# Optimization experiments

Hardware: AMD Instinct MI355X
Metric: run time of the kernel (lower is better)

## Reference

```python
import jax, jax.numpy as jnp
import numpy as np

H, W, C = 384, 384, 200
HIDE, CNN_OUT, NCLS = 128, 64, 16
N = H * W
E = 1179648
EPS = 1e-5  # torch BatchNorm eps


def _bn(x, g, b, axes):
    # training-mode batch norm (biased variance), matches torch BN in train mode
    m = x.mean(axes, keepdims=True)
    v = x.var(axes, keepdims=True)
    return (x - m) * jax.lax.rsqrt(v + EPS) * g + b


def _gcn(x, w, bias, src, dst, n):
    # PyG GCNConv: add self loops, symmetric D^-1/2 (A+I) D^-1/2 normalization
    h = x @ w  # [N, out]
    loop = jnp.arange(n, dtype=src.dtype)
    s = jnp.concatenate([src, loop])
    d = jnp.concatenate([dst, loop])
    deg = jax.ops.segment_sum(jnp.ones(s.shape, x.dtype), d, num_segments=n)
    dinv = jnp.where(deg > 0, jax.lax.rsqrt(jnp.maximum(deg, 1.0)) * (deg > 0), 0.0)
    norm = dinv[s] * dinv[d]  # [E+N]
    out = jax.ops.segment_sum(h[s] * norm[:, None], d, num_segments=n)
    return out + bias


def _gnn_layer(x, bn_g, bn_b, w, b, src, dst):
    # F.normalize (row L2) -> BN1d -> GCNConv -> LeakyReLU (dropout off in eval)
    nrm = jnp.linalg.norm(x, axis=1, keepdims=True)
    x = x / jnp.maximum(nrm, 1e-12)
    x = _bn(x, bn_g, bn_b, (0,))
    return jax.nn.leaky_relu(_gcn(x, w, b, src, dst, x.shape[0]))


def setup_inputs() -> dict:
    key = jax.random.key(0)
    ks = jax.random.split(key, 16)
    p = {}
    p["x"] = jax.random.normal(ks[0], (H, W, C), jnp.float32)
    p["edge_index"] = jax.random.randint(ks[1], (2, E), 0, N, jnp.int32)
    # CNN_denoise: BN(C) -> 1x1 conv C->128 -> BN(128) -> 1x1 conv 128->128
    p["dn_bn1_g"] = jnp.ones((C,), jnp.float32); p["dn_bn1_b"] = jnp.zeros((C,), jnp.float32)
    p["dn_w1"] = jax.random.normal(ks[2], (C, HIDE), jnp.float32) * 0.05
    p["dn_b1"] = jnp.zeros((HIDE,), jnp.float32)
    p["dn_bn2_g"] = jnp.ones((HIDE,), jnp.float32); p["dn_bn2_b"] = jnp.zeros((HIDE,), jnp.float32)
    p["dn_w2"] = jax.random.normal(ks[3], (HIDE, HIDE), jnp.float32) * 0.05
    p["dn_b2"] = jnp.zeros((HIDE,), jnp.float32)
    # CNNCONV(128,64,k=5): BN(128) -> point 1x1 128->64 (no bias) -> depthwise 5x5 (bias)
    p["cnn_bn_g"] = jnp.ones((HIDE,), jnp.float32); p["cnn_bn_b"] = jnp.zeros((HIDE,), jnp.float32)
    p["cnn_pw"] = jax.random.normal(ks[4], (HIDE, CNN_OUT), jnp.float32) * 0.05
    p["cnn_dw"] = jax.random.normal(ks[5], (CNN_OUT, 1, 5, 5), jnp.float32) * 0.05
    p["cnn_db"] = jnp.zeros((CNN_OUT,), jnp.float32)
    # GCN branch: GNN(128,128), GNN(128,128), GNN(128,64)
    dims = [(HIDE, HIDE), (HIDE, HIDE), (HIDE, CNN_OUT)]
    for i, (di, do) in enumerate(dims, 1):
        p[f"g{i}_bn_g"] = jnp.ones((di,), jnp.float32)
        p[f"g{i}_bn_b"] = jnp.zeros((di,), jnp.float32)
        p[f"g{i}_w"] = jax.random.normal(ks[5 + i], (di, do), jnp.float32) * 0.05
        p[f"g{i}_b"] = jnp.zeros((do,), jnp.float32)
    p["lin_w"] = jax.random.normal(ks[9], (HIDE, NCLS), jnp.float32) * 0.05
    p["lin_b"] = jnp.zeros((NCLS,), jnp.float32)
    return p


def reference(x, edge_index,
              dn_bn1_g, dn_bn1_b, dn_w1, dn_b1, dn_bn2_g, dn_bn2_b, dn_w2, dn_b2,
              cnn_bn_g, cnn_bn_b, cnn_pw, cnn_dw, cnn_db,
              g1_bn_g, g1_bn_b, g1_w, g1_b,
              g2_bn_g, g2_bn_b, g2_w, g2_b,
              g3_bn_g, g3_bn_b, g3_w, g3_b,
              lin_w, lin_b):
    src, dst = edge_index[0], edge_index[1]
    # CNN_denoise (channel-last; 1x1 convs are matmuls)
    h = _bn(x, dn_bn1_g, dn_bn1_b, (0, 1))
    h = jax.nn.leaky_relu(h @ dn_w1 + dn_b1)
    h = _bn(h, dn_bn2_g, dn_bn2_b, (0, 1))
    clean = jax.nn.leaky_relu(h @ dn_w2 + dn_b2)       # [H,W,128]
    flat = clean.reshape(N, HIDE)
    # CNN branch: BN -> 1x1 -> LeakyReLU -> depthwise 5x5 -> LeakyReLU
    c = _bn(clean, cnn_bn_g, cnn_bn_b, (0, 1))
    c = jax.nn.leaky_relu(c @ cnn_pw)                  # [H,W,64]
    cn = c.transpose(2, 0, 1)[None]                    # [1,64,H,W]
    cn = jax.lax.conv_general_dilated(
        cn, cnn_dw, (1, 1), 'SAME', feature_group_count=CNN_OUT,
        dimension_numbers=('NCHW', 'OIHW', 'NCHW'))
    cn = jax.nn.leaky_relu(cn[0].transpose(1, 2, 0) + cnn_db)
    cnn_res = cn.reshape(N, CNN_OUT)
    # GCN branch (3 layers)
    g = _gnn_layer(flat, g1_bn_g, g1_bn_b, g1_w, g1_b, src, dst)
    g = _gnn_layer(g, g2_bn_g, g2_bn_b, g2_w, g2_b, src, dst)
    g = _gnn_layer(g, g3_bn_g, g3_bn_b, g3_w, g3_b, src, dst)
    y = jnp.concatenate([g, cnn_res], axis=-1) @ lin_w + lin_b
    return jax.nn.softmax(y, axis=-1)
```

## Files before the change

### kernel.cpp

```cpp
#include <hip/hip_runtime.h>
#include <stddef.h>

#define HH 384
#define WW 384
#define CC 200
#define NN 147456
#define EE 1179648
#define HIDE 128
#define COUT 64
#define NCLS 16
#define BN_EPS 1e-5f

#define SREP 16
#define SLOTF (512 * SREP)
#define DBINS 64

using u16 = unsigned short;
typedef __attribute__((ext_vector_type(8))) short short8;
typedef __attribute__((ext_vector_type(4))) float float4v;

__device__ __forceinline__ float b2f(u16 u) {
    union { unsigned int i; float f; } v; v.i = ((unsigned int)u) << 16; return v.f;
}
__device__ __forceinline__ u16 f2b(float f) {
    union { float f; unsigned int i; } v; v.f = f;
    unsigned int x = v.i;
    unsigned int r = (x + 0x7fffu + ((x >> 16) & 1u)) >> 16;
    return (u16)r;
}
__device__ __forceinline__ float lrelu(float v) { return v > 0.f ? v : 0.01f * v; }

__global__ void sniff(const u16* __restrict__ x, int* __restrict__ flag) {
    __shared__ int cntS;
    if (threadIdx.x == 0) cntS = 0;
    __syncthreads();
    int c = 0;
    for (int i = 0; i < 8; i++) {
        u16 h = x[threadIdx.x * 8 + i];
        int hb = (h >> 8) & 0x7F;
        if (hb >= 0x3C && hb <= 0x41) c++;
    }
    atomicAdd(&cntS, c);
    __syncthreads();
    if (threadIdx.x == 0) *flag = (cntS < 1536) ? 1 : 0;
}

#define NPAR 27
struct PConv { const void* src[NPAR]; int n[NPAR]; int off[NPAR]; };

__global__ void convert_params(PConv pc, const int* __restrict__ flag,
                               u16* __restrict__ dst) {
    int b = blockIdx.x;
    int n = pc.n[b];
    const void* s = pc.src[b];
    u16* d = dst + pc.off[b];
    int isf = *flag;
    if (isf) {
        const float* sf = (const float*)s;
        for (int i = threadIdx.x; i < n; i += 256) d[i] = f2b(sf[i]);
    } else {
        const u16* sh = (const u16*)s;
        for (int i = threadIdx.x; i < n; i += 256) d[i] = sh[i];
    }
}

__global__ __launch_bounds__(256) void stats200(const void* __restrict__ X,
                                                const int* __restrict__ flag,
                                                float* __restrict__ arena) {
    __shared__ __align__(16) u16 s[128 * 200];
    int t = threadIdx.x;
    int r0 = blockIdx.x * 128;
    if (*flag) {
        const float* Xf = (const float*)X;
        for (int i = t; i < 128 * 25; i += 256) {
            int r = i / 25, kc = i - r * 25;
            const float* p = Xf + (size_t)(r0 + r) * CC + kc * 8;
            float4v a = *(const float4v*)p;
            float4v b = *(const float4v*)(p + 4);
            short8 v;
            #pragma unroll
            for (int j = 0; j < 4; j++) { v[j] = (short)f2b(a[j]); v[4 + j] = (short)f2b(b[j]); }
            *(short8*)&s[r * 200 + kc * 8] = v;
        }
    } else {
        const u16* Xh = (const u16*)X;
        for (int i = t; i < 128 * 25; i += 256) {
            int r = i / 25, kc = i - r * 25;
            *(short8*)&s[r * 200 + kc * 8] =
                *(const short8*)(Xh + (size_t)(r0 + r) * CC + kc * 8);
        }
    }
    __syncthreads();
    if (t < CC) {
        float sum = 0.f, sq = 0.f;
        for (int r = 0; r < 128; r++) {
            float v = b2f(s[r * 200 + t]);
            sum += v; sq += v * v;
        }
        float* rep = arena + (blockIdx.x & (SREP - 1)) * 512;
        atomicAdd(&rep[t], sum);
        atomicAdd(&rep[256 + t], sq);
    }
}

template<int K, int KPAD, int O>
__global__ __launch_bounds__(256) void fold_bn(
        const float* __restrict__ arena, float invN,
        const u16* __restrict__ bng, const u16* __restrict__ bnb,
        const u16* __restrict__ Wsrc, const u16* __restrict__ extrab,
        u16* __restrict__ WT, float* __restrict__ cb) {
    __shared__ float aS[KPAD], sS[KPAD];
    int t = threadIdx.x;
    if (t < KPAD) {
        float a = 0.f, sh = 0.f;
        if (t < K) {
            float sum = 0.f, sq = 0.f;
            #pragma unroll
            for (int r = 0; r < SREP; r++) {
                sum += arena[r * 512 + t];
                sq  += arena[r * 512 + 256 + t];
            }
            float m = sum * invN;
            float var = fmaxf(sq * invN - m * m, 0.f);
            a = b2f(bng[t]) * rsqrtf(var + BN_EPS);
            sh = b2f(bnb[t]) - m * a;
        }
        aS[t] = a; sS[t] = sh;
    }
    __syncthreads();
    int g = t >> 6, l = t & 63;
    int o = blockIdx.x * 4 + g;
    if (o < O) {
        float c = 0.f;
        #pragma unroll
        for (int k = l; k < KPAD; k += 64) {
            float w = (k < K) ? b2f(Wsrc[k * O + o]) : 0.f;
            c += sS[k] * w;
            WT[o * KPAD + k] = f2b(aS[k] * w);
        }
        #pragma unroll
        for (int s = 32; s >= 1; s >>= 1) c += __shfl_down(c, s);
        if (l == 0) cb[o] = c + (extrab ? b2f(extrab[o]) : 0.f);
    }
}

template<int KT, int KSRC, int O, bool LEAKY, bool SCALE, int STATS, bool DUAL>
__global__ __launch_bounds__(256) void gemm_mfma(
        const void* __restrict__ Ap, const u16* __restrict__ WT,
        const float* __restrict__ cb, const float* __restrict__ s1,
        const float* __restrict__ s2, const int* __restrict__ f32p,
        u16* __restrict__ out, float* __restrict__ stA,
        float* __restrict__ stB, float* __restrict__ invn,
        u16* __restrict__ out2) {
    constexpr int KPAD = KT * 32;
    constexpr int LDA = KPAD + 8;
    constexpr int CHR = KPAD / 8;
    constexpr int CHD = KSRC / 8;
    constexpr int NCT = O / 16;
    constexpr int CPW = NCT / 4;
    __shared__ __align__(16) u16 As[64 * LDA];
    __shared__ float rS[4][64];
    __shared__ float invS[64];
    __shared__ float sS1[64], sS2[64];
    int tid = threadIdx.x;
    int row0 = blockIdx.x * 64;

    int isf = f32p ? *f32p : 0;
    if (isf) {
        const float* A = (const float*)Ap;
        for (int i = tid; i < 64 * CHR; i += 256) {
            int r = i / CHR, kc = i - r * CHR;
            short8 v = {0, 0, 0, 0, 0, 0, 0, 0};
            if (kc < CHD) {
                const float* p = A + (size_t)(row0 + r) * KSRC + kc * 8;
                float4v a = *(const float4v*)p;
                float4v b = *(const float4v*)(p + 4);
                #pragma unroll
                for (int j = 0; j < 4; j++) { v[j] = (short)f2b(a[j]); v[4 + j] = (short)f2b(b[j]); }
            }
            *(short8*)&As[r * LDA + kc * 8] = v;
        }
    } else {
        const u16* A = (const u16*)Ap;
        for (int i = tid; i < 64 * CHR; i += 256) {
            int r = i / CHR, kc = i - r * CHR;
            short8 v = {0, 0, 0, 0, 0, 0, 0, 0};
            if (kc < CHD)
                v = *(const short8*)(A + (size_t)(row0 + r) * KSRC + kc * 8);
            *(short8*)&As[r * LDA + kc * 8] = v;
        }
    }
    if (SCALE && tid < 64) { sS1[tid] = s1[row0 + tid]; sS2[tid] = s2[row0 + tid]; }
    __syncthreads();

    int w = tid >> 6, lane = tid & 63, m = lane & 15, q = lane >> 4;
    float4v acc[4][CPW];
    #pragma unroll
    for (int mf = 0; mf < 4; mf++)
        #pragma unroll
        for (int cp = 0; cp < CPW; cp++)
            acc[mf][cp] = (float4v){0.f, 0.f, 0.f, 0.f};

    const u16* Abp = &As[m * LDA + q * 8];
    const u16* Bbp = WT + (size_t)((w * CPW) * 16 + m) * KPAD + q * 8;

    #pragma unroll
    for (int kt = 0; kt < KT; kt++) {
        short8 af[4];
        #pragma unroll
        for (int mf = 0; mf < 4; mf++)
            af[mf] = *(const short8*)(Abp + mf * 16 * LDA + kt * 32);
        #pragma unroll
        for (int cp = 0; cp < CPW; cp++) {
            short8 bf = *(const short8*)(Bbp + (size_t)cp * 16 * KPAD + kt * 32);
            #pragma unroll
            for (int mf = 0; mf < 4; mf++)
                acc[mf][cp] = __builtin_amdgcn_mfma_f32_16x16x32_bf16(
                    af[mf], bf, acc[mf][cp], 0, 0, 0);
        }
    }

    float rp[4][4] = {};
    #pragma unroll
    for (int cp = 0; cp < CPW; cp++) {
        int ct = w * CPW + cp;
        int col = ct * 16 + m;
        float cbv = cb[col];
        #pragma unroll
        for (int mf = 0; mf < 4; mf++) {
            #pragma unroll
            for (int r = 0; r < 4; r++) {
                int rl = mf * 16 + q * 4 + r;
                float x = acc[mf][cp][r];
                if constexpr (DUAL) {
                    if (ct < 8) {
                        x = (x * sS1[rl] + cbv) * sS2[rl];
                        out[(size_t)(row0 + rl) * 128 + col] = f2b(x);
                    } else {
                        x = lrelu(x + cbv);
                        out2[(size_t)(row0 + rl) * 64 + (col - 128)] = f2b(x);
                    }
                } else {
                    if constexpr (SCALE) x = (x * sS1[rl] + cbv) * sS2[rl];
                    else                 x += cbv;
                    if constexpr (LEAKY) x = lrelu(x);
                    out[(size_t)(row0 + rl) * O + col] = f2b(x);
                }
                acc[mf][cp][r] = x;
                if constexpr (STATS == 2) rp[mf][r] += x * x;
            }
        }
    }

    if constexpr (STATS == 2) {
        #pragma unroll
        for (int mf = 0; mf < 4; mf++) {
            #pragma unroll
            for (int r = 0; r < 4; r++) {
                float v = rp[mf][r];
                v += __shfl_xor(v, 1); v += __shfl_xor(v, 2);
                v += __shfl_xor(v, 4); v += __shfl_xor(v, 8);
                if (m == 0) rS[w][mf * 16 + q * 4 + r] = v;
            }
        }
        __syncthreads();
        if (tid < 64) {
            float ss = rS[0][tid] + rS[1][tid] + rS[2][tid] + rS[3][tid];
            float inv = 1.0f / fmaxf(sqrtf(ss), 1e-12f);
            invS[tid] = inv;
            invn[row0 + tid] = inv;
        }
        __syncthreads();
    }

    if constexpr (STATS >= 1) {
        float* stAr = stA + (blockIdx.x & (SREP - 1)) * 512;
        float* stBr = (STATS == 2) ? stB + (blockIdx.x & (SREP - 1)) * 512 : nullptr;
        #pragma unroll
        for (int cp = 0; cp < CPW; cp++) {
            int col = (w * CPW + cp) * 16 + m;
            float cs = 0.f, cq = 0.f, ns = 0.f, nq = 0.f;
            #pragma unroll
            for (int mf = 0; mf < 4; mf++) {
                #pragma unroll
                for (int r = 0; r < 4; r++) {
                    float x = acc[mf][cp][r];
                    cs += x; cq += x * x;
                    if constexpr (STATS == 2) {
                        float nv = x * invS[mf * 16 + q * 4 + r];
                        ns += nv; nq += nv * nv;
                    }
                }
            }
            cs += __shfl_xor(cs, 16); cs += __shfl_xor(cs, 32);
            cq += __shfl_xor(cq, 16); cq += __shfl_xor(cq, 32);
            if constexpr (STATS == 2) {
                ns += __shfl_xor(ns, 16); ns += __shfl_xor(ns, 32);
                nq += __shfl_xor(nq, 16); nq += __shfl_xor(nq, 32);
            }
            if (q == 0) {
                atomicAdd(&stAr[col], cs);
                atomicAdd(&stAr[256 + col], cq);
                if constexpr (STATS == 2) {
                    atomicAdd(&stBr[col], ns);
                    atomicAdd(&stBr[256 + col], nq);
                }
            }
        }
    }
}

__global__ void hist(const int* __restrict__ dst, int* __restrict__ cnt) {
    int e = blockIdx.x * 256 + threadIdx.x;
    unsigned d = (unsigned)dst[e];
    if (d < (unsigned)NN) atomicAdd(&cnt[d], 1);
}
__global__ void mkdinv(const int* __restrict__ cnt, float* __restrict__ dinv) {
    int i = blockIdx.x * 256 + threadIdx.x;
    int c = cnt[i]; if (c < 0) c = 0;
    dinv[i] = rsqrtf((float)c + 1.0f);
}
__global__ void scan_part(const int* __restrict__ cnt, int* __restrict__ bsum) {
    int b = blockIdx.x, t = threadIdx.x;
    int base = b * 1024 + t * 4;
    int s = cnt[base] + cnt[base + 1] + cnt[base + 2] + cnt[base + 3];
    #pragma unroll
    for (int o = 32; o >= 1; o >>= 1) s += __shfl_down(s, o);
    __shared__ int ws4[4];
    if ((t & 63) == 0) ws4[t >> 6] = s;
    __syncthreads();
    if (t == 0) bsum[b] = ws4[0] + ws4[1] + ws4[2] + ws4[3];
}
__global__ void scan_top(const int* __restrict__ bsum, int* __restrict__ boff) {
    if (threadIdx.x == 0) {
        int a = 0;
        for (int i = 0; i < 144; i++) { boff[i] = a; a += bsum[i]; }
    }
}
__global__ void scan_write(const int* __restrict__ cnt, const int* __restrict__ boff,
                           int* __restrict__ offv) {
    int b = blockIdx.x, t = threadIdx.x;
    int base = b * 1024 + t * 4;
    int v0 = cnt[base], v1 = cnt[base + 1], v2 = cnt[base + 2], v3 = cnt[base + 3];
    int ts = v0 + v1 + v2 + v3;
    __shared__ int sc[256];
    sc[t] = ts;
    __syncthreads();
    for (int o = 1; o < 256; o <<= 1) {
        int x = (t >= o) ? sc[t - o] : 0;
        __syncthreads();
        sc[t] += x;
        __syncthreads();
    }
    int excl = boff[b] + sc[t] - ts;
    offv[base] = excl;
    offv[base + 1] = excl + v0;
    offv[base + 2] = excl + v0 + v1;
    offv[base + 3] = excl + v0 + v1 + v2;
    if (b == 143 && t == 255) offv[NN] = excl + ts;
}
__global__ void scatter(const int* __restrict__ src, const int* __restrict__ dst,
                        int* __restrict__ cursor, const int* __restrict__ offv,
                        int* __restrict__ csr) {
    int e = blockIdx.x * 256 + threadIdx.x;
    unsigned d = (unsigned)dst[e];
    if (d >= (unsigned)NN) return;
    int p = atomicAdd(&cursor[d], 1);
    unsigned idx = (unsigned)(offv[d] + p);
    if (idx < (unsigned)EE) csr[idx] = src[e];
}

__global__ void deg_hist(const int* __restrict__ cnt, int* __restrict__ dbin) {
    __shared__ int h[DBINS];
    int t = threadIdx.x;
    if (t < DBINS) h[t] = 0;
    __syncthreads();
    int i = blockIdx.x * 256 + t;
    int dg = cnt[i]; if (dg < 0) dg = 0; if (dg > DBINS - 1) dg = DBINS - 1;
    atomicAdd(&h[dg], 1);
    __syncthreads();
    if (t < DBINS) atomicAdd(&dbin[t], h[t]);
}
__global__ void deg_scan(const int* __restrict__ dbin, int* __restrict__ dbase) {
    if (threadIdx.x == 0) {
        int a = 0;
        for (int b = DBINS - 1; b >= 0; b--) { dbase[b] = a; a += dbin[b]; }
    }
}
__global__ void deg_scatter(const int* __restrict__ cnt, int* __restrict__ dbase,
                            int* __restrict__ perm) {
    __shared__ int h[DBINS], base[DBINS];
    int t = threadIdx.x;
    if (t < DBINS) h[t] = 0;
    __syncthreads();
    int i = blockIdx.x * 256 + t;
    int dg = cnt[i]; if (dg < 0) dg = 0; if (dg > DBINS - 1) dg = DBINS - 1;
    atomicAdd(&h[dg], 1);
    __syncthreads();
    if (t < DBINS) { base[t] = atomicAdd(&dbase[t], h[t]); h[t] = 0; }
    __syncthreads();
    int lp = atomicAdd(&h[dg], 1);
    perm[base[dg] + lp] = i;
}

template<int O, int STATS, int GRP>
__global__ __launch_bounds__(256) void aggregate(
        const u16* __restrict__ h2, const int* __restrict__ offv,
        const int* __restrict__ csr, const float* __restrict__ dinv,
        const u16* __restrict__ gb, u16* __restrict__ outp,
        float* __restrict__ stA, float* __restrict__ invn,
        const int* __restrict__ perm) {
    constexpr int CH = O / 8;
    constexpr int NPB = 256 / CH;
    __shared__ float colS[O], colQ[O];
    int t = threadIdx.x;
    if (STATS && t < O) { colS[t] = 0.f; colQ[t] = 0.f; }
    int local = t / CH, c = t % CH;
    size_t cof = (size_t)c * 8;
    const u16* hb = h2 + cof;
    short8 gv = *(const short8*)(gb + cof);
    float sreg[8] = {0.f, 0.f, 0.f, 0.f, 0.f, 0.f, 0.f, 0.f};
    float qreg[8] = {0.f, 0.f, 0.f, 0.f, 0.f, 0.f, 0.f, 0.f};

    #pragma unroll
    for (int g = 0; g < GRP; g++) {
        int pos = blockIdx.x * (NPB * GRP) + g * NPB + local;
        int d = perm[pos];
        float acc[8];
        short8 selfv = *(const short8*)(hb + (size_t)d * O);
        #pragma unroll
        for (int j = 0; j < 8; j++) acc[j] = b2f((u16)selfv[j]);
        int e0 = offv[d], e1 = offv[d + 1];
        if (e0 < 0) e0 = 0;
        if (e1 > EE) e1 = EE;
        int k = e0;
        for (; k + 8 <= e1; k += 8) {
            unsigned i0 = (unsigned)csr[k],     i1 = (unsigned)csr[k + 1];
            unsigned i2 = (unsigned)csr[k + 2], i3 = (unsigned)csr[k + 3];
            unsigned i4 = (unsigned)csr[k + 4], i5 = (unsigned)csr[k + 5];
            unsigned i6 = (unsigned)csr[k + 6], i7 = (unsigned)csr[k + 7];
            short8 v0 = *(const short8*)(hb + (size_t)i0 * O);
            short8 v1 = *(const short8*)(hb + (size_t)i1 * O);
            short8 v2 = *(const short8*)(hb + (size_t)i2 * O);
            short8 v3 = *(const short8*)(hb + (size_t)i3 * O);
            short8 v4 = *(const short8*)(hb + (size_t)i4 * O);
            short8 v5 = *(const short8*)(hb + (size_t)i5 * O);
            short8 v6 = *(const short8*)(hb + (size_t)i6 * O);
            short8 v7 = *(const short8*)(hb + (size_t)i7 * O);
            #pragma unroll
            for (int j = 0; j < 8; j++)
                acc[j] += ((b2f((u16)v0[j]) + b2f((u16)v1[j])) +
                           (b2f((u16)v2[j]) + b2f((u16)v3[j]))) +
                          ((b2f((u16)v4[j]) + b2f((u16)v5[j])) +
                           (b2f((u16)v6[j]) + b2f((u16)v7[j])));
        }
        if (k + 4 <= e1) {
            unsigned i0 = (unsigned)csr[k],     i1 = (unsigned)csr[k + 1];
            unsigned i2 = (unsigned)csr[k + 2], i3 = (unsigned)csr[k + 3];
            short8 v0 = *(const short8*)(hb + (size_t)i0 * O);
            short8 v1 = *(const short8*)(hb + (size_t)i1 * O);
            short8 v2 = *(const short8*)(hb + (size_t)i2 * O);
            short8 v3 = *(const short8*)(hb + (size_t)i3 * O);
            #pragma unroll
            for (int j = 0; j < 8; j++)
                acc[j] += (b2f((u16)v0[j]) + b2f((u16)v1[j])) +
                          (b2f((u16)v2[j]) + b2f((u16)v3[j]));
            k += 4;
        }
        if (k + 2 <= e1) {
            unsigned i0 = (unsigned)csr[k], i1 = (unsigned)csr[k + 1];
            short8 v0 = *(const short8*)(hb + (size_t)i0 * O);
            short8 v1 = *(const short8*)(hb + (size_t)i1 * O);
            #pragma unroll
            for (int j = 0; j < 8; j++)
                acc[j] += b2f((u16)v0[j]) + b2f((u16)v1[j]);
            k += 2;
        }
        if (k < e1) {
            unsigned i0 = (unsigned)csr[k];
            short8 v0 = *(const short8*)(hb + (size_t)i0 * O);
            #pragma unroll
            for (int j = 0; j < 8; j++) acc[j] += b2f((u16)v0[j]);
        }
        float dd = dinv[d];
        float outv[8];
        short8 res;
        #pragma unroll
        for (int j = 0; j < 8; j++) {
            outv[j] = lrelu(dd * acc[j] + b2f((u16)gv[j]));
            res[j] = (short)f2b(outv[j]);
        }
        *(short8*)(outp + (size_t)d * O + cof) = res;

        if constexpr (STATS) {
            float ss = 0.f;
            #pragma unroll
            for (int j = 0; j < 8; j++) ss += outv[j] * outv[j];
            ss += __shfl_xor(ss, 1); ss += __shfl_xor(ss, 2);
            ss += __shfl_xor(ss, 4); ss += __shfl_xor(ss, 8);
            float inv = 1.0f / fmaxf(sqrtf(ss), 1e-12f);
            if (c == 0) invn[d] = inv;
            #pragma unroll
            for (int j = 0; j < 8; j++) {
                float nv = outv[j] * inv;
                sreg[j] += nv; qreg[j] += nv * nv;
            }
        }
    }

    if constexpr (STATS) {
        __syncthreads();
        #pragma unroll
        for (int j = 0; j < 8; j++) {
            float s = sreg[j];
            s += __shfl_xor(s, 16); s += __shfl_xor(s, 32);
            float qq = qreg[j];
            qq += __shfl_xor(qq, 16); qq += __shfl_xor(qq, 32);
            if ((t & 63) < 16) {
                atomicAdd(&colS[c * 8 + j], s);
                atomicAdd(&colQ[c * 8 + j], qq);
            }
        }
        __syncthreads();
        if (t < O) {
            float* rep = stA + (blockIdx.x & (SREP - 1)) * 512;
            atomicAdd(&rep[t], colS[t]);
            atomicAdd(&rep[256 + t], colQ[t]);
        }
    }
}

__global__ __launch_bounds__(256) void final_fused(
        const u16* __restrict__ g3, const u16* __restrict__ cpre,
        const u16* __restrict__ dwW, const u16* __restrict__ db,
        const u16* __restrict__ lw, const u16* __restrict__ lb,
        const int* __restrict__ flag, void* __restrict__ outp) {
    __shared__ __align__(16) u16 tile[400 * 72];
    __shared__ __align__(16) u16 wT[25 * 64];
    __shared__ __align__(16) u16 wL[2048];
    __shared__ float bDW[64];
    __shared__ float bL[16];
    int t = threadIdx.x;
    int tx = blockIdx.x % 24, ty = blockIdx.x / 24;
    int x0 = tx * 16 - 2, y0 = ty * 16 - 2;
    for (int i = t; i < 1600; i += 256) {
        int f = i / 25, tap = i - f * 25;
        wT[tap * 64 + f] = dwW[i];
    }
    for (int i = t; i < 2048; i += 256) wL[i] = lw[i];
    if (t < 64) bDW[t] = b2f(db[t]);
    if (t < 16) bL[t] = b2f(lb[t]);
    for (int u = t; u < 3200; u += 256) {
        int pix = u >> 3, c8 = u & 7;
        int gy = y0 + pix / 20, gx = x0 + pix % 20;
        short8 v = {0, 0, 0, 0, 0, 0, 0, 0};
        if (gy >= 0 && gy < HH && gx >= 0 && gx < WW)
            v = *(const short8*)(cpre + ((size_t)(gy * WW + gx)) * 64 + c8 * 8);
        *(short8*)&tile[pix * 72 + c8 * 8] = v;
    }
    __syncthreads();

    int px = t & 15, py = t >> 4;
    int node = (ty * 16 + py) * WW + tx * 16 + px;
    float y[16];
    #pragma unroll
    for (int o = 0; o < 16; o++) y[o] = bL[o];

    const u16* g3p = g3 + (size_t)node * 64;
    for (int c8 = 0; c8 < 8; c8++) {
        short8 gvv = *(const short8*)(g3p + c8 * 8);
        #pragma unroll
        for (int j = 0; j < 8; j++) {
            float g = b2f((u16)gvv[j]);
            const short8 w0 = *(const short8*)&wL[(c8 * 8 + j) * 16];
            const short8 w1 = *(const short8*)&wL[(c8 * 8 + j) * 16 + 8];
            #pragma unroll
            for (int o = 0; o < 8; o++) {
                y[o]     += g * b2f((u16)w0[o]);
                y[o + 8] += g * b2f((u16)w1[o]);
            }
        }
    }
    for (int c8 = 0; c8 < 8; c8++) {
        float acc[8] = {0.f, 0.f, 0.f, 0.f, 0.f, 0.f, 0.f, 0.f};
        #pragma unroll
        for (int dy = 0; dy < 5; dy++) {
            int rbase = ((py + dy) * 20 + px) * 72 + c8 * 8;
            #pragma unroll
            for (int dx = 0; dx < 5; dx++) {
                short8 v  = *(const short8*)&tile[rbase + dx * 72];
                short8 wv = *(const short8*)&wT[(dy * 5 + dx) * 64 + c8 * 8];
                #pragma unroll
                for (int j = 0; j < 8; j++)
                    acc[j] += b2f((u16)v[j]) * b2f((u16)wv[j]);
            }
        }
        #pragma unroll
        for (int j = 0; j < 8; j++) {
            float cv = lrelu(acc[j] + bDW[c8 * 8 + j]);
            int f = 64 + c8 * 8 + j;
            const short8 w0 = *(const short8*)&wL[f * 16];
            const short8 w1 = *(const short8*)&wL[f * 16 + 8];
            #pragma unroll
            for (int o = 0; o < 8; o++) {
                y[o]     += cv * b2f((u16)w0[o]);
                y[o + 8] += cv * b2f((u16)w1[o]);
            }
        }
    }
    float mx = y[0];
    #pragma unroll
    for (int o = 1; o < 16; o++) mx = fmaxf(mx, y[o]);
    float sum = 0.f;
    #pragma unroll
    for (int o = 0; o < 16; o++) { y[o] = __expf(y[o] - mx); sum += y[o]; }
    float inv = 1.0f / fmaxf(sum, 1e-30f);
    if (*flag) {
        float* of = (float*)outp;
        #pragma unroll
        for (int o = 0; o < 16; o++) of[(size_t)node * 16 + o] = y[o] * inv;
    } else {
        u16* oh = (u16*)outp;
        #pragma unroll
        for (int o = 0; o < 16; o++) oh[(size_t)node * 16 + o] = f2b(y[o] * inv);
    }
}

extern "C" void kernel_launch(void* const* d_in, const int* in_sizes, int n_in,
                              void* d_out, int out_size, void* d_ws, size_t ws_size,
                              hipStream_t stream) {
    const void* X   = d_in[0];
    const int* EIDX = (const int*)d_in[1];
    const int* esrc = EIDX;
    const int* edst = EIDX + EE;

    char* ws = (char*)d_ws;
    size_t off = 0;
    auto alloc = [&](size_t sz) -> char* {
        size_t szr = (sz + 255) & ~(size_t)255;
        char* p;
        if (off + szr <= ws_size) { p = ws + off; off += szr; }
        else { p = ws; }
        return p;
    };

    int*   dflag   = (int*)alloc(256);
    static const int pidx[NPAR] = {2,3,4,5,6,7,8,9,10,11,12,13,14,
                                   15,16,17,18,19,20,21,22,23,24,25,26,27,28};
    static const int pn[NPAR]   = {200,200,25600,128,128,128,16384,128,
                                   128,128,8192,1600,64,
                                   128,128,16384,128,
                                   128,128,16384,128,
                                   128,128,8192,64,
                                   2048,16};
    u16* parena = (u16*)alloc(100352 * 2);
    PConv pc;
    {
        int po = 0;
        for (int i = 0; i < NPAR; i++) {
            pc.src[i] = d_in[pidx[i]];
            pc.n[i] = pn[i];
            pc.off[i] = po;
            po += (pn[i] + 15) & ~15;
        }
    }
    const u16* DN1G = parena + pc.off[0];
    const u16* DN1B = parena + pc.off[1];
    const u16* DNW1 = parena + pc.off[2];
    const u16* DNB1 = parena + pc.off[3];
    const u16* DN2G = parena + pc.off[4];
    const u16* DN2B = parena + pc.off[5];
    const u16* DNW2 = parena + pc.off[6];
    const u16* DNB2 = parena + pc.off[7];
    const u16* CBNG = parena + pc.off[8];
    const u16* CBNB = parena + pc.off[9];
    const u16* CPW  = parena + pc.off[10];
    const u16* CDW  = parena + pc.off[11];
    const u16* CDB  = parena + pc.off[12];
    const u16* G1G  = parena + pc.off[13];
    const u16* G1B  = parena + pc.off[14];
    const u16* G1W  = parena + pc.off[15];
    const u16* G1BI = parena + pc.off[16];
    const u16* G2G  = parena + pc.off[17];
    const u16* G2B  = parena + pc.off[18];
    const u16* G2W  = parena + pc.off[19];
    const u16* G2BI = parena + pc.off[20];
    const u16* G3G  = parena + pc.off[21];
    const u16* G3B  = parena + pc.off[22];
    const u16* G3W  = parena + pc.off[23];
    const u16* G3BI = parena + pc.off[24];
    const u16* LINW = parena + pc.off[25];
    const u16* LINB = parena + pc.off[26];

    int*   cnt     = (int*)alloc((size_t)NN * 4);
    int*   cursor  = (int*)alloc((size_t)NN * 4);
    float* arena   = (float*)alloc((size_t)6 * SLOTF * 4);
    int*   dbin    = (int*)alloc(DBINS * 4);
    int*   offv    = (int*)alloc((size_t)(NN + 1) * 4);
    int*   bsum    = (int*)alloc(144 * 4);
    int*   boff    = (int*)alloc(144 * 4);
    int*   dbase   = (int*)alloc(DBINS * 4);
    int*   perm    = (int*)alloc((size_t)NN * 4);
    float* dinvp   = (float*)alloc((size_t)NN * 4);
    float* invnorm = (float*)alloc((size_t)NN * 4);
    u16*   W1T     = (u16*)alloc(128 * 224 * 2);
    u16*   W2T     = (u16*)alloc(128 * 128 * 2);
    u16*   WgT     = (u16*)alloc(192 * 128 * 2);
    float* cb1     = (float*)alloc(128 * 4);
    float* cb2     = (float*)alloc(128 * 4);
    float* cbg     = (float*)alloc(192 * 4);
    int*   csr     = (int*)alloc((size_t)EE * 4);
    u16*   cbuf    = (u16*)alloc((size_t)NN * 64 * 2);
    u16*   big1    = (u16*)alloc((size_t)NN * 128 * 2);
    u16*   big2    = (u16*)alloc((size_t)NN * 128 * 2);

    const float invN = 1.0f / (float)NN;
    size_t zsz = (size_t)((char*)dbin + 256 - (char*)cnt);
    size_t zcap = ((char*)cnt >= ws && (size_t)((char*)cnt - ws) < ws_size)
                      ? ws_size - (size_t)((char*)cnt - ws) : 0;
    if (zsz > zcap) zsz = zcap;
    hipMemsetAsync(cnt, 0, zsz, stream);

    sniff<<<1, 256, 0, stream>>>((const u16*)X, dflag);
    convert_params<<<NPAR, 256, 0, stream>>>(pc, dflag, parena);

    hist<<<EE / 256, 256, 0, stream>>>(edst, cnt);
    mkdinv<<<NN / 256, 256, 0, stream>>>(cnt, dinvp);
    deg_hist<<<NN / 256, 256, 0, stream>>>(cnt, dbin);
    deg_scan<<<1, 64, 0, stream>>>(dbin, dbase);
    deg_scatter<<<NN / 256, 256, 0, stream>>>(cnt, dbase, perm);
    scan_part<<<144, 256, 0, stream>>>(cnt, bsum);
    scan_top<<<1, 64, 0, stream>>>(bsum, boff);
    scan_write<<<144, 256, 0, stream>>>(cnt, boff, offv);
    scatter<<<EE / 256, 256, 0, stream>>>(esrc, edst, cursor, offv, csr);

    stats200<<<1152, 256, 0, stream>>>(X, dflag, arena + 0 * SLOTF);
    fold_bn<200, 224, 128><<<32, 256, 0, stream>>>(arena + 0 * SLOTF, invN, DN1G, DN1B, DNW1, DNB1, W1T, cb1);
    gemm_mfma<7, 200, 128, true, false, 1, false><<<NN / 64, 256, 0, stream>>>(
        X, W1T, cb1, nullptr, nullptr, dflag, big1, arena + 1 * SLOTF, nullptr, nullptr, nullptr);
    fold_bn<128, 128, 128><<<32, 256, 0, stream>>>(arena + 1 * SLOTF, invN, DN2G, DN2B, DNW2, DNB2, W2T, cb2);
    gemm_mfma<4, 128, 128, true, false, 2, false><<<NN / 64, 256, 0, stream>>>(
        big1, W2T, cb2, nullptr, nullptr, nullptr, big2, arena + 2 * SLOTF, arena + 3 * SLOTF, invnorm, nullptr);

    fold_bn<128, 128, 128><<<32, 256, 0, stream>>>(arena + 3 * SLOTF, invN, G1G, G1B, G1W, nullptr, WgT, cbg);
    fold_bn<128, 128, 64><<<16, 256, 0, stream>>>(arena + 2 * SLOTF, invN, CBNG, CBNB, CPW, nullptr,
                                                  WgT + 128 * 128, cbg + 128);
    gemm_mfma<4, 128, 192, false, true, 0, true><<<NN / 64, 256, 0, stream>>>(
        big2, WgT, cbg, invnorm, dinvp, nullptr, big1, nullptr, nullptr, nullptr, cbuf);
    aggregate<128, 1, 4><<<NN / 64, 256, 0, stream>>>(
        big1, offv, csr, dinvp, G1BI, big2, arena + 4 * SLOTF, invnorm, perm);

    fold_bn<128, 128, 128><<<32, 256, 0, stream>>>(arena + 4 * SLOTF, invN, G2G, G2B, G2W, nullptr, WgT, cbg);
    gemm_mfma<4, 128, 128, false, true, 0, false><<<NN / 64, 256, 0, stream>>>(
        big2, WgT, cbg, invnorm, dinvp, nullptr, big1, nullptr, nullptr, nullptr, nullptr);
    aggregate<128, 1, 4><<<NN / 64, 256, 0, stream>>>(
        big1, offv, csr, dinvp, G2BI, big2, arena + 5 * SLOTF, invnorm, perm);

    fold_bn<128, 128, 64><<<16, 256, 0, stream>>>(arena + 5 * SLOTF, invN, G3G, G3B, G3W, nullptr, WgT, cbg);
    gemm_mfma<4, 128, 64, false, true, 0, false><<<NN / 64, 256, 0, stream>>>(
        big2, WgT, cbg, invnorm, dinvp, nullptr, big1, nullptr, nullptr, nullptr, nullptr);
    aggregate<64, 0, 1><<<NN / 32, 256, 0, stream>>>(
        big1, offv, csr, dinvp, G3BI, big2, nullptr, nullptr, perm);

    final_fused<<<576, 256, 0, stream>>>(big2, cbuf, CDW, CDB, LINW, LINB, dflag, d_out);

    (void)in_sizes; (void)n_in; (void)out_size;
}
```

Before: 798.7 us.

## Build CSR via two-level bucket partition with LDS-local counting instead of global atomics

Replaces the global-atomic histogram, three-kernel scan and global-atomic scatter with a bucketed counting sort. Edges are first partitioned by destination into 72 buckets of 2048 nodes using per-block shared-memory counters, then each bucket builds its CSR offsets and column lists with LDS atomics. Degrees for dinv and the degree-sort permutation are derived from offset differences. This removes contended global atomics and random global writes, but adds an 8-byte-per-edge intermediate pass, and csr_build runs as only 72 blocks, which limits parallelism.

Result: faster. 760.1 us (-4.8%).

```diff
diff --git a/kernel.cpp b/kernel.cpp
--- a/kernel.cpp
+++ b/kernel.cpp
@@ -14,6 +14,10 @@
 #define SREP 16
 #define SLOTF (512 * SREP)
 #define DBINS 64
+
+#define NBKT 72
+#define NPBK 288
+#define EPB  4096
 
 using u16 = unsigned short;
 typedef __attribute__((ext_vector_type(8))) short short8;
@@ -310,73 +314,122 @@
     }
 }
 
-__global__ void hist(const int* __restrict__ dst, int* __restrict__ cnt) {
-    int e = blockIdx.x * 256 + threadIdx.x;
-    unsigned d = (unsigned)dst[e];
-    if (d < (unsigned)NN) atomicAdd(&cnt[d], 1);
-}
-__global__ void mkdinv(const int* __restrict__ cnt, float* __restrict__ dinv) {
+__global__ __launch_bounds__(256) void count_bkt(const int* __restrict__ edst,
+                                                 int* __restrict__ counts) {
+    __shared__ int h[NBKT];
+    int t = threadIdx.x, blk = blockIdx.x;
+    if (t < NBKT) h[t] = 0;
+    __syncthreads();
+    int base = blk * EPB;
+    for (int i = t; i < EPB; i += 256) {
+        unsigned d = (unsigned)edst[base + i];
+        if (d < (unsigned)NN) atomicAdd(&h[d >> 11], 1);
+    }
+    __syncthreads();
+    if (t < NBKT) counts[t * NPBK + blk] = h[t];
+}
+
+__global__ void scan_bkt(int* __restrict__ counts, int* __restrict__ bbase) {
+    __shared__ int bs[NBKT], bb[NBKT];
+    int t = threadIdx.x;
+    if (t < NBKT) {
+        int s = 0;
+        for (int i = 0; i < NPBK; i++) s += counts[t * NPBK + i];
+        bs[t] = s;
+    }
+    __syncthreads();
+    if (t == 0) {
+        int a = 0;
+        for (int b = 0; b < NBKT; b++) { bb[b] = a; bbase[b] = a; a += bs[b]; }
+        bbase[NBKT] = a;
+    }
+    __syncthreads();
+    if (t < NBKT) {
+        int run = bb[t];
+        for (int i = 0; i < NPBK; i++) {
+            int c = counts[t * NPBK + i];
+            counts[t * NPBK + i] = run;
+            run += c;
+        }
+    }
+}
+
+__global__ __launch_bounds__(256) void part_bkt(const int* __restrict__ esrc,
+                                                const int* __restrict__ edst,
+                                                const int* __restrict__ counts,
+                                                int2* __restrict__ bpair) {
+    __shared__ int cur[NBKT];
+    int t = threadIdx.x, blk = blockIdx.x;
+    if (t < NBKT) cur[t] = counts[t * NPBK + blk];
+    __syncthreads();
+    int base = blk * EPB;
+    for (int i = t; i < EPB; i += 256) {
+        unsigned d = (unsigned)edst[base + i];
+        if (d < (unsigned)NN) {
+            int pos = atomicAdd(&cur[d >> 11], 1);
+            int2 p; p.x = esrc[base + i]; p.y = (int)d;
+            bpair[pos] = p;
+        }
+    }
+}
+
+__global__ __launch_bounds__(256) void csr_build(const int2* __restrict__ bpair,
+                                                 const int* __restrict__ bbase,
+                                                 int* __restrict__ offv,
+                                                 int* __restrict__ csr) {
+    __shared__ int cntL[2048];
+    __shared__ int exL[2048];
+    __shared__ int tsum[256];
+    int b = blockIdx.x, t = threadIdx.x;
+    int e0 = bbase[b], e1 = bbase[b + 1];
+    int n0 = b << 11;
+    for (int i = t; i < 2048; i += 256) cntL[i] = 0;
+    __syncthreads();
+    for (int k = e0 + t; k < e1; k += 256) {
+        int2 p = bpair[k];
+        atomicAdd(&cntL[p.y & 2047], 1);
+    }
+    __syncthreads();
+    int s = 0;
+    #pragma unroll
+    for (int j = 0; j < 8; j++) s += cntL[t * 8 + j];
+    tsum[t] = s;
+    __syncthreads();
+    for (int o = 1; o < 256; o <<= 1) {
+        int x = (t >= o) ? tsum[t - o] : 0;
+        __syncthreads();
+        tsum[t] += x;
+        __syncthreads();
+    }
+    int run = tsum[t] - s;
+    #pragma unroll
+    for (int j = 0; j < 8; j++) { int c = cntL[t * 8 + j]; exL[t * 8 + j] = run; run += c; }
+    __syncthreads();
+    for (int i = t; i < 2048; i += 256) offv[n0 + i] = e0 + exL[i];
+    if (b == NBKT - 1 && t == 0) offv[NN] = e1;
+    for (int i = t; i < 2048; i += 256) cntL[i] = 0;
+    __syncthreads();
+    for (int k = e0 + t; k < e1; k += 256) {
+        int2 p = bpair[k];
+        int l = p.y & 2047;
+        int pos = e0 + exL[l] + atomicAdd(&cntL[l], 1);
+        csr[pos] = p.x;
+    }
+}
+
+__global__ void mkdinv2(const int* __restrict__ offv, float* __restrict__ dinv) {
     int i = blockIdx.x * 256 + threadIdx.x;
-    int c = cnt[i]; if (c < 0) c = 0;
-    dinv[i] = rsqrtf((float)c + 1.0f);
-}
-__global__ void scan_part(const int* __restrict__ cnt, int* __restrict__ bsum) {
-    int b = blockIdx.x, t = threadIdx.x;
-    int base = b * 1024 + t * 4;
-    int s = cnt[base] + cnt[base + 1] + cnt[base + 2] + cnt[base + 3];
-    #pragma unroll
-    for (int o = 32; o >= 1; o >>= 1) s += __shfl_down(s, o);
-    __shared__ int ws4[4];
-    if ((t & 63) == 0) ws4[t >> 6] = s;
-    __syncthreads();
-    if (t == 0) bsum[b] = ws4[0] + ws4[1] + ws4[2] + ws4[3];
-}
-__global__ void scan_top(const int* __restrict__ bsum, int* __restrict__ boff) {
-    if (threadIdx.x == 0) {
-        int a = 0;
-        for (int i = 0; i < 144; i++) { boff[i] = a; a += bsum[i]; }
-    }
-}
-__global__ void scan_write(const int* __restrict__ cnt, const int* __restrict__ boff,
-                           int* __restrict__ offv) {
-    int b = blockIdx.x, t = threadIdx.x;
-    int base = b * 1024 + t * 4;
-    int v0 = cnt[base], v1 = cnt[base + 1], v2 = cnt[base + 2], v3 = cnt[base + 3];
-    int ts = v0 + v1 + v2 + v3;
-    __shared__ int sc[256];
-    sc[t] = ts;
-    __syncthreads();
-    for (int o = 1; o < 256; o <<= 1) {
-        int x = (t >= o) ? sc[t - o] : 0;
-        __syncthreads();
-        sc[t] += x;
-        __syncthreads();
-    }
-    int excl = boff[b] + sc[t] - ts;
-    offv[base] = excl;
-    offv[base + 1] = excl + v0;
-    offv[base + 2] = excl + v0 + v1;
-    offv[base + 3] = excl + v0 + v1 + v2;
-    if (b == 143 && t == 255) offv[NN] = excl + ts;
-}
-__global__ void scatter(const int* __restrict__ src, const int* __restrict__ dst,
-                        int* __restrict__ cursor, const int* __restrict__ offv,
-                        int* __restrict__ csr) {
-    int e = blockIdx.x * 256 + threadIdx.x;
-    unsigned d = (unsigned)dst[e];
-    if (d >= (unsigned)NN) return;
-    int p = atomicAdd(&cursor[d], 1);
-    unsigned idx = (unsigned)(offv[d] + p);
-    if (idx < (unsigned)EE) csr[idx] = src[e];
-}
-
-__global__ void deg_hist(const int* __restrict__ cnt, int* __restrict__ dbin) {
+    dinv[i] = rsqrtf((float)(offv[i + 1] - offv[i]) + 1.0f);
+}
+
+__global__ void deg_hist(const int* __restrict__ offv, int* __restrict__ dbin) {
     __shared__ int h[DBINS];
     int t = threadIdx.x;
     if (t < DBINS) h[t] = 0;
     __syncthreads();
     int i = blockIdx.x * 256 + t;
-    int dg = cnt[i]; if (dg < 0) dg = 0; if (dg > DBINS - 1) dg = DBINS - 1;
+    int dg = offv[i + 1] - offv[i];
+    if (dg < 0) dg = 0; if (dg > DBINS - 1) dg = DBINS - 1;
     atomicAdd(&h[dg], 1);
     __syncthreads();
     if (t < DBINS) atomicAdd(&dbin[t], h[t]);
@@ -387,14 +440,15 @@
         for (int b = DBINS - 1; b >= 0; b--) { dbase[b] = a; a += dbin[b]; }
     }
 }
-__global__ void deg_scatter(const int* __restrict__ cnt, int* __restrict__ dbase,
+__global__ void deg_scatter(const int* __restrict__ offv, int* __restrict__ dbase,
                             int* __restrict__ perm) {
     __shared__ int h[DBINS], base[DBINS];
     int t = threadIdx.x;
     if (t < DBINS) h[t] = 0;
     __syncthreads();
     int i = blockIdx.x * 256 + t;
-    int dg = cnt[i]; if (dg < 0) dg = 0; if (dg > DBINS - 1) dg = DBINS - 1;
+    int dg = offv[i + 1] - offv[i];
+    if (dg < 0) dg = 0; if (dg > DBINS - 1) dg = DBINS - 1;
     atomicAdd(&h[dg], 1);
     __syncthreads();
     if (t < DBINS) { base[t] = atomicAdd(&dbase[t], h[t]); h[t] = 0; }
@@ -692,13 +746,12 @@
     const u16* LINW = parena + pc.off[25];
     const u16* LINB = parena + pc.off[26];
 
-    int*   cnt     = (int*)alloc((size_t)NN * 4);
-    int*   cursor  = (int*)alloc((size_t)NN * 4);
     float* arena   = (float*)alloc((size_t)6 * SLOTF * 4);
     int*   dbin    = (int*)alloc(DBINS * 4);
+    int*   counts  = (int*)alloc((size_t)NBKT * NPBK * 4);
+    int*   bbase   = (int*)alloc((NBKT + 1) * 4);
+    int2*  bpair   = (int2*)alloc((size_t)EE * 8);
     int*   offv    = (int*)alloc((size_t)(NN + 1) * 4);
-    int*   bsum    = (int*)alloc(144 * 4);
-    int*   boff    = (int*)alloc(144 * 4);
     int*   dbase   = (int*)alloc(DBINS * 4);
     int*   perm    = (int*)alloc((size_t)NN * 4);
     float* dinvp   = (float*)alloc((size_t)NN * 4);
@@ -715,24 +768,23 @@
     u16*   big2    = (u16*)alloc((size_t)NN * 128 * 2);
 
     const float invN = 1.0f / (float)NN;
-    size_t zsz = (size_t)((char*)dbin + 256 - (char*)cnt);
-    size_t zcap = ((char*)cnt >= ws && (size_t)((char*)cnt - ws) < ws_size)
-                      ? ws_size - (size_t)((char*)cnt - ws) : 0;
+    size_t zsz = (size_t)((char*)dbin + 256 - (char*)arena);
+    size_t zcap = ((char*)arena >= ws && (size_t)((char*)arena - ws) < ws_size)
+                      ? ws_size - (size_t)((char*)arena - ws) : 0;
     if (zsz > zcap) zsz = zcap;
-    hipMemsetAsync(cnt, 0, zsz, stream);
+    hipMemsetAsync(arena, 0, zsz, stream);
 
     sniff<<<1, 256, 0, stream>>>((const u16*)X, dflag);
     convert_params<<<NPAR, 256, 0, stream>>>(pc, dflag, parena);
 
-    hist<<<EE / 256, 256, 0, stream>>>(edst, cnt);
-    mkdinv<<<NN / 256, 256, 0, stream>>>(cnt, dinvp);
-    deg_hist<<<NN / 256, 256, 0, stream>>>(cnt, dbin);
+    count_bkt<<<NPBK, 256, 0, stream>>>(edst, counts);
+    scan_bkt<<<1, 128, 0, stream>>>(counts, bbase);
+    part_bkt<<<NPBK, 256, 0, stream>>>(esrc, edst, counts, bpair);
+    csr_build<<<NBKT, 256, 0, stream>>>(bpair, bbase, offv, csr);
+    mkdinv2<<<NN / 256, 256, 0, stream>>>(offv, dinvp);
+    deg_hist<<<NN / 256, 256, 0, stream>>>(offv, dbin);
     deg_scan<<<1, 64, 0, stream>>>(dbin, dbase);
-    deg_scatter<<<NN / 256, 256, 0, stream>>>(cnt, dbase, perm);
-    scan_part<<<144, 256, 0, stream>>>(cnt, bsum);
-    scan_top<<<1, 64, 0, stream>>>(bsum, boff);
-    scan_write<<<144, 256, 0, stream>>>(cnt, boff, offv);
-    scatter<<<EE / 256, 256, 0, stream>>>(esrc, edst, cursor, offv, csr);
+    deg_scatter<<<NN / 256, 256, 0, stream>>>(offv, dbase, perm);
 
     stats200<<<1152, 256, 0, stream>>>(X, dflag, arena + 0 * SLOTF);
     fold_bn<200, 224, 128><<<32, 256, 0, stream>>>(arena + 0 * SLOTF, invN, DN1G, DN1B, DNW1, DNB1, W1T, cb1);
```
